# Kernel optimization log

Hardware: AMD Instinct MI355X
Metric: run time of the kernel (lower is better)

The kernel has to match this reference:

```python
import jax, jax.numpy as jnp
import numpy as np

E = 64          # num_experts
D_IN = 512      # in_features
D_OUT = 512     # out_features
T = 262144      # total routed token-slots (grouped by expert, balanced)


def setup_inputs() -> dict:
    key = jax.random.key(0)
    k1, k2 = jax.random.split(key)
    STD = 0.02
    return {
        "input": jax.random.normal(k1, (T, D_IN), dtype=jnp.float32),
        # tokens are pre-grouped by expert; balanced routing -> equal counts
        "num_experts_per_token": jnp.full((E,), T // E, dtype=jnp.int64),
        "weight": jax.random.normal(k2, (E, D_OUT, D_IN), dtype=jnp.float32) * STD,
        "bias": jnp.zeros((E, D_OUT), dtype=jnp.float32),
    }


def reference(input, num_experts_per_token, weight, bias):
    # Faithful to the split + per-expert F.linear + cat path, for balanced
    # routing (equal counts per expert) so shapes are static under jit.
    e = weight.shape[0]
    tpe = input.shape[0] // e  # tokens per expert
    x = input.reshape(e, tpe, -1)                      # [E, tpe, D_in]
    # F.linear(x_e, W_e) = x_e @ W_e.T for each expert -> grouped GEMM
    out = jnp.einsum('eti,eoi->eto', x, weight)        # [E, tpe, D_out]
    out = out + bias[:, None, :]
    return out.reshape(e * tpe, -1)                    # [T, D_out]
```

## Files before the change

### kernel.cpp

```cpp
#include <hip/hip_runtime.h>
#include <hip/hip_bf16.h>


#define NEXPERT 64
#define DIN 512
#define DOUT 512
#define TPE 4096
#define BM 256
#define BN 128
#define BK 32
#define NKT (DIN / BK)

typedef __attribute__((ext_vector_type(8))) __bf16 bf16x8;
typedef __attribute__((ext_vector_type(4))) __bf16 bf16x4;
typedef __attribute__((ext_vector_type(4))) float f32x4;

#define BAR()     asm volatile("s_barrier" ::: "memory")
#define BAR_PUB() asm volatile("s_waitcnt lgkmcnt(0)\n\ts_barrier" ::: "memory")

__global__ __launch_bounds__(512, 2)
void moe_grouped_gemm(const float* __restrict__ x,
                      const float* __restrict__ w,
                      const float* __restrict__ bias,
                      float* __restrict__ out) {
  __shared__ __align__(16) unsigned char sA[2][BM * BK * 2];
  __shared__ __align__(16) unsigned char sB[2][BN * BK * 2];

  int bid = blockIdx.x;
  int swz = (bid & 7) * 512 + (bid >> 3);
  int e  = swz >> 6;
  int rr = swz & 63;
  int mt = rr >> 2;
  int nt = rr & 3;

  const int tid  = threadIdx.x;
  const int lane = tid & 63;
  const int wave = tid >> 6;
  const int wm   = wave >> 1;
  const int wn   = wave & 1;
  const int r15  = lane & 15;
  const int kg   = lane >> 4;

  const int c4  = tid & 7;
  const int gr0 = tid >> 3;
  const float* aG = x + ((size_t)e * TPE + (size_t)mt * BM + gr0) * DIN + c4 * 4;
  const float* bG = w + ((size_t)e * DOUT + (size_t)nt * BN + gr0) * DIN + c4 * 4;
  const int swzByte = (((c4 >> 1) ^ ((tid >> 4) & 3)) << 4) + (c4 & 1) * 8;

  const int chA = (kg ^ ((r15 >> 1) & 3)) << 4;
  const int aFrag0 = (wm * 64 + r15) * 64 + chA;
  const int bFrag0 = (wn * 64 + r15) * 64 + chA;

  f32x4 A0[4], B0[2], A1[4], B1[2];

#define ISSUE(kt, Ar, Br)                                                   \
  do {                                                                      \
    _Pragma("unroll") for (int i = 0; i < 4; ++i)                           \
      Ar[i] = *(const f32x4*)(aG + (size_t)i * 64 * DIN + (kt) * BK);       \
    _Pragma("unroll") for (int i = 0; i < 2; ++i)                           \
      Br[i] = *(const f32x4*)(bG + (size_t)i * 64 * DIN + (kt) * BK);       \
  } while (0)

#define WRITE(dbuf, Ar, Br)                                                 \
  do {                                                                      \
    _Pragma("unroll") for (int i = 0; i < 4; ++i) {                         \
      bf16x4 c;                                                             \
      c[0] = (__bf16)Ar[i][0]; c[1] = (__bf16)Ar[i][1];                     \
      c[2] = (__bf16)Ar[i][2]; c[3] = (__bf16)Ar[i][3];                     \
      *(bf16x4*)(&sA[dbuf][(i * 64 + gr0) * 64 + swzByte]) = c;             \
    }                                                                       \
    _Pragma("unroll") for (int i = 0; i < 2; ++i) {                         \
      bf16x4 c;                                                             \
      c[0] = (__bf16)Br[i][0]; c[1] = (__bf16)Br[i][1];                     \
      c[2] = (__bf16)Br[i][2]; c[3] = (__bf16)Br[i][3];                     \
      *(bf16x4*)(&sB[dbuf][(i * 64 + gr0) * 64 + swzByte]) = c;             \
    }                                                                       \
  } while (0)

  f32x4 acc[4][4];
#pragma unroll
  for (int m = 0; m < 4; ++m)
#pragma unroll
    for (int n = 0; n < 4; ++n) acc[m][n] = (f32x4)0.f;

  ISSUE(0, A0, B0);
  ISSUE(1, A1, B1);
  WRITE(0, A0, B0);
  BAR_PUB();

#pragma unroll
  for (int t = 0; t < NKT; ++t) {
    const int d = t & 1;
    bf16x8 af[4], bfr[4];
#pragma unroll
    for (int mi = 0; mi < 4; ++mi)
      af[mi] = *(const bf16x8*)(&sA[d][aFrag0 + mi * 1024]);
#pragma unroll
    for (int ni = 0; ni < 4; ++ni)
      bfr[ni] = *(const bf16x8*)(&sB[d][bFrag0 + ni * 1024]);

    if ((t & 1) == 0) {
      if (t + 2 < NKT) ISSUE(t + 2, A0, B0);
      if (t + 1 < NKT) WRITE(d ^ 1, A1, B1);
    } else {
      if (t + 2 < NKT) ISSUE(t + 2, A1, B1);
      if (t + 1 < NKT) WRITE(d ^ 1, A0, B0);
    }

    BAR();
    __builtin_amdgcn_s_setprio(1);
#pragma unroll
    for (int mi = 0; mi < 4; ++mi)
#pragma unroll
      for (int ni = 0; ni < 4; ++ni)
        acc[mi][ni] = __builtin_amdgcn_mfma_f32_16x16x32_bf16(
            af[mi], bfr[ni], acc[mi][ni], 0, 0, 0);
    __builtin_amdgcn_s_setprio(0);
    BAR_PUB();
  }

  float bv[4];
  const float* bp = bias + (size_t)e * DOUT + nt * BN + wn * 64 + r15;
#pragma unroll
  for (int n = 0; n < 4; ++n) bv[n] = bp[n * 16];

  const int q4 = (lane >> 4) * 4;
  float* Cb = out + ((size_t)e * TPE + (size_t)mt * BM + wm * 64) * DOUT
              + nt * BN + wn * 64;
#pragma unroll
  for (int m = 0; m < 4; ++m) {
#pragma unroll
    for (int j = 0; j < 4; ++j) {
      float* pr = Cb + (size_t)(m * 16 + q4 + j) * DOUT;
#pragma unroll
      for (int n = 0; n < 4; ++n)
        pr[n * 16 + r15] = acc[m][n][j] + bv[n];
    }
  }
#undef ISSUE
#undef WRITE
}

extern "C" void kernel_launch(void* const* d_in, const int* in_sizes, int n_in,
                              void* d_out, int out_size, void* d_ws, size_t ws_size,
                              hipStream_t stream) {
  const float* x    = (const float*)d_in[0];
  const float* w    = (const float*)d_in[2];
  const float* bias = (const float*)d_in[3];
  float* out        = (float*)d_out;

  dim3 grid(NEXPERT * (TPE / BM) * (DOUT / BN));
  dim3 block(512);
  hipLaunchKernelGGL(moe_grouped_gemm, grid, block, 0, stream, x, w, bias, out);
}
```

Baseline: 328.5 us.

## Retile to 128x256 with four waves and split-phase A fragment loads

Changes the block tile from 256x128 to 128x256 and cuts the block from eight waves to four, so each wave covers a 128x64 output tile (8x4 MFMA accumulators). Register double-buffering of the global prefetch is replaced by a single prefetch stage. Each k-step is split into two MFMA halves, with the upper A fragments loaded and the next tile written to LDS between them. The aim is more MFMA work per wave and per LDS fragment load, plus interleaving the LDS writes with compute. The cost is more accumulator registers, fewer waves to hide latency, and extra barriers per iteration.

```diff
diff --git a/kernel.cpp b/kernel.cpp
--- a/kernel.cpp
+++ b/kernel.cpp
@@ -6,8 +6,8 @@
 #define DIN 512
 #define DOUT 512
 #define TPE 4096
-#define BM 256
-#define BN 128
+#define BM 128
+#define BN 256
 #define BK 32
 #define NKT (DIN / BK)
 
@@ -15,10 +15,7 @@
 typedef __attribute__((ext_vector_type(4))) __bf16 bf16x4;
 typedef __attribute__((ext_vector_type(4))) float f32x4;
 
-#define BAR()     asm volatile("s_barrier" ::: "memory")
-#define BAR_PUB() asm volatile("s_waitcnt lgkmcnt(0)\n\ts_barrier" ::: "memory")
-
-__global__ __launch_bounds__(512, 2)
+__global__ __launch_bounds__(256, 2)
 void moe_grouped_gemm(const float* __restrict__ x,
                       const float* __restrict__ w,
                       const float* __restrict__ bias,
@@ -30,93 +27,102 @@
   int swz = (bid & 7) * 512 + (bid >> 3);
   int e  = swz >> 6;
   int rr = swz & 63;
-  int mt = rr >> 2;
-  int nt = rr & 3;
+  int mt = rr >> 1;
+  int nt = rr & 1;
 
   const int tid  = threadIdx.x;
   const int lane = tid & 63;
-  const int wave = tid >> 6;
-  const int wm   = wave >> 1;
-  const int wn   = wave & 1;
+  const int wn   = tid >> 6;
   const int r15  = lane & 15;
   const int kg   = lane >> 4;
 
-  const int c4  = tid & 7;
-  const int gr0 = tid >> 3;
-  const float* aG = x + ((size_t)e * TPE + (size_t)mt * BM + gr0) * DIN + c4 * 4;
-  const float* bG = w + ((size_t)e * DOUT + (size_t)nt * BN + gr0) * DIN + c4 * 4;
-  const int swzByte = (((c4 >> 1) ^ ((tid >> 4) & 3)) << 4) + (c4 & 1) * 8;
+  const int c4 = tid & 7;
+  const int tr = tid >> 3;
+  const float* aG = x + ((size_t)e * TPE + (size_t)mt * BM + tr) * DIN + c4 * 4;
+  const float* bG = w + ((size_t)e * DOUT + (size_t)nt * BN + tr) * DIN + c4 * 4;
+  const int wrBase = tr * 64 + ((((c4 >> 1) ^ ((tr >> 1) & 3))) << 4) + (c4 & 1) * 8;
 
-  const int chA = (kg ^ ((r15 >> 1) & 3)) << 4;
-  const int aFrag0 = (wm * 64 + r15) * 64 + chA;
-  const int bFrag0 = (wn * 64 + r15) * 64 + chA;
+  const int chz = (kg ^ ((r15 >> 1) & 3)) << 4;
+  const int aRd = r15 * 64 + chz;
+  const int bRd = (wn * 64 + r15) * 64 + chz;
 
-  f32x4 A0[4], B0[2], A1[4], B1[2];
+  f32x4 SA[4], SBv[8];
 
-#define ISSUE(kt, Ar, Br)                                                   \
+#define ISSUE(kt)                                                           \
   do {                                                                      \
     _Pragma("unroll") for (int i = 0; i < 4; ++i)                           \
-      Ar[i] = *(const f32x4*)(aG + (size_t)i * 64 * DIN + (kt) * BK);       \
-    _Pragma("unroll") for (int i = 0; i < 2; ++i)                           \
-      Br[i] = *(const f32x4*)(bG + (size_t)i * 64 * DIN + (kt) * BK);       \
+      SA[i] = *(const f32x4*)(aG + (size_t)i * 32 * DIN + (kt) * BK);       \
+    _Pragma("unroll") for (int i = 0; i < 8; ++i)                           \
+      SBv[i] = *(const f32x4*)(bG + (size_t)i * 32 * DIN + (kt) * BK);      \
   } while (0)
 
-#define WRITE(dbuf, Ar, Br)                                                 \
+#define WRITE(dbuf)                                                         \
   do {                                                                      \
     _Pragma("unroll") for (int i = 0; i < 4; ++i) {                         \
       bf16x4 c;                                                             \
-      c[0] = (__bf16)Ar[i][0]; c[1] = (__bf16)Ar[i][1];                     \
-      c[2] = (__bf16)Ar[i][2]; c[3] = (__bf16)Ar[i][3];                     \
-      *(bf16x4*)(&sA[dbuf][(i * 64 + gr0) * 64 + swzByte]) = c;             \
+      c[0] = (__bf16)SA[i][0]; c[1] = (__bf16)SA[i][1];                     \
+      c[2] = (__bf16)SA[i][2]; c[3] = (__bf16)SA[i][3];                     \
+      *(bf16x4*)(&sA[dbuf][wrBase + i * 2048]) = c;                         \
     }                                                                       \
-    _Pragma("unroll") for (int i = 0; i < 2; ++i) {                         \
+    _Pragma("unroll") for (int i = 0; i < 8; ++i) {                         \
       bf16x4 c;                                                             \
-      c[0] = (__bf16)Br[i][0]; c[1] = (__bf16)Br[i][1];                     \
-      c[2] = (__bf16)Br[i][2]; c[3] = (__bf16)Br[i][3];                     \
-      *(bf16x4*)(&sB[dbuf][(i * 64 + gr0) * 64 + swzByte]) = c;             \
+      c[0] = (__bf16)SBv[i][0]; c[1] = (__bf16)SBv[i][1];                   \
+      c[2] = (__bf16)SBv[i][2]; c[3] = (__bf16)SBv[i][3];                   \
+      *(bf16x4*)(&sB[dbuf][wrBase + i * 2048]) = c;                         \
     }                                                                       \
   } while (0)
 
-  f32x4 acc[4][4];
+  f32x4 acc[8][4];
 #pragma unroll
-  for (int m = 0; m < 4; ++m)
+  for (int m = 0; m < 8; ++m)
 #pragma unroll
     for (int n = 0; n < 4; ++n) acc[m][n] = (f32x4)0.f;
 
-  ISSUE(0, A0, B0);
-  ISSUE(1, A1, B1);
-  WRITE(0, A0, B0);
-  BAR_PUB();
+  ISSUE(0);
+  WRITE(0);
+  asm volatile("s_waitcnt lgkmcnt(0)" ::: "memory");
+  __builtin_amdgcn_s_barrier();
 
 #pragma unroll
   for (int t = 0; t < NKT; ++t) {
     const int d = t & 1;
-    bf16x8 af[4], bfr[4];
+    bf16x8 bfr[4], afl[4], afh[4];
+
+#pragma unroll
+    for (int ni = 0; ni < 4; ++ni)
+      bfr[ni] = *(const bf16x8*)(&sB[d][bRd + ni * 1024]);
 #pragma unroll
     for (int mi = 0; mi < 4; ++mi)
-      af[mi] = *(const bf16x8*)(&sA[d][aFrag0 + mi * 1024]);
-#pragma unroll
-    for (int ni = 0; ni < 4; ++ni)
-      bfr[ni] = *(const bf16x8*)(&sB[d][bFrag0 + ni * 1024]);
+      afl[mi] = *(const bf16x8*)(&sA[d][aRd + mi * 1024]);
+    if (t + 1 < NKT) ISSUE(t + 1);
 
-    if ((t & 1) == 0) {
-      if (t + 2 < NKT) ISSUE(t + 2, A0, B0);
-      if (t + 1 < NKT) WRITE(d ^ 1, A1, B1);
-    } else {
-      if (t + 2 < NKT) ISSUE(t + 2, A1, B1);
-      if (t + 1 < NKT) WRITE(d ^ 1, A0, B0);
-    }
-
-    BAR();
+    __builtin_amdgcn_s_barrier();
     __builtin_amdgcn_s_setprio(1);
 #pragma unroll
     for (int mi = 0; mi < 4; ++mi)
 #pragma unroll
       for (int ni = 0; ni < 4; ++ni)
         acc[mi][ni] = __builtin_amdgcn_mfma_f32_16x16x32_bf16(
-            af[mi], bfr[ni], acc[mi][ni], 0, 0, 0);
+            afl[mi], bfr[ni], acc[mi][ni], 0, 0, 0);
     __builtin_amdgcn_s_setprio(0);
-    BAR_PUB();
+    __builtin_amdgcn_s_barrier();
+
+#pragma unroll
+    for (int mi = 0; mi < 4; ++mi)
+      afh[mi] = *(const bf16x8*)(&sA[d][aRd + 4096 + mi * 1024]);
+    if (t + 1 < NKT) WRITE(d ^ 1);
+
+    asm volatile("s_waitcnt lgkmcnt(0)" ::: "memory");
+    __builtin_amdgcn_s_barrier();
+    __builtin_amdgcn_s_setprio(1);
+#pragma unroll
+    for (int mi = 0; mi < 4; ++mi)
+#pragma unroll
+      for (int ni = 0; ni < 4; ++ni)
+        acc[mi + 4][ni] = __builtin_amdgcn_mfma_f32_16x16x32_bf16(
+            afh[mi], bfr[ni], acc[mi + 4][ni], 0, 0, 0);
+    __builtin_amdgcn_s_setprio(0);
+    __builtin_amdgcn_s_barrier();
   }
 
   float bv[4];
@@ -125,10 +131,9 @@
   for (int n = 0; n < 4; ++n) bv[n] = bp[n * 16];
 
   const int q4 = (lane >> 4) * 4;
-  float* Cb = out + ((size_t)e * TPE + (size_t)mt * BM + wm * 64) * DOUT
-              + nt * BN + wn * 64;
+  float* Cb = out + ((size_t)e * TPE + (size_t)mt * BM) * DOUT + nt * BN + wn * 64;
 #pragma unroll
-  for (int m = 0; m < 4; ++m) {
+  for (int m = 0; m < 8; ++m) {
 #pragma unroll
     for (int j = 0; j < 4; ++j) {
       float* pr = Cb + (size_t)(m * 16 + q4 + j) * DOUT;
@@ -150,6 +155,6 @@
   float* out        = (float*)d_out;
 
   dim3 grid(NEXPERT * (TPE / BM) * (DOUT / BN));
-  dim3 block(512);
+  dim3 block(256);
   hipLaunchKernelGGL(moe_grouped_gemm, grid, block, 0, stream, x, w, bias, out);
 }
```

After: 305.3 us. -7.1%, faster.
